# Optimization experiments

Hardware: AMD Instinct MI355X
Metric: run time of the kernel (lower is better)

Reference implementation:

```python
import jax, jax.numpy as jnp
import numpy as np

N_HEAD = 16
LN_EPS = 1e-5


def _rope_tables(T, hd, dtype):
    # Standard GPT-NeoX style rotary tables: cos/sin of shape [T, hd]
    inv = 1.0 / (10000.0 ** (np.arange(0, hd, 2, dtype=np.float64) / hd))
    freqs = np.outer(np.arange(T), inv)
    emb = np.concatenate([freqs, freqs], axis=-1)
    return jnp.asarray(np.cos(emb), dtype), jnp.asarray(np.sin(emb), dtype)


def _rotate_half(x):
    x1, x2 = jnp.split(x, 2, axis=-1)
    return jnp.concatenate([-x2, x1], axis=-1)


def _layernorm(x, g, b):
    mu = x.mean(-1, keepdims=True)
    var = x.var(-1, keepdims=True)
    return (x - mu) / jnp.sqrt(var + LN_EPS) * g + b


def _heads(x, H):
    B, T, C = x.shape
    return x.reshape(B, T, H, C // H).transpose(0, 2, 1, 3)  # [B,H,T,hd]


def _lin_attention(Q, K, V, causal):
    # Q,K,V: [B,H,T,hd]; ELU+1 feature map, RoPE on features, denom = sum_s Q.K
    Qf = jax.nn.elu(Q) + 1.0
    Kf = jax.nn.elu(K) + 1.0
    hd = Qf.shape[-1]
    cq, sq = _rope_tables(Qf.shape[2], hd, Qf.dtype)
    ck, sk = _rope_tables(Kf.shape[2], hd, Kf.dtype)
    Qr = Qf * cq + _rotate_half(Qf) * sq
    Kr = Kf * ck + _rotate_half(Kf) * sk
    # denom.sum(-1) == Qf . (sum_s Kf) -- avoid materializing a second TxS matrix
    denom = jnp.einsum('bhtd,bhd->bht', Qf, Kf.sum(axis=2))[..., None]
    att = jnp.einsum('bhtd,bhsd->bhts', Qr, Kr)
    if causal:
        T, S = att.shape[-2], att.shape[-1]
        att = jnp.where(jnp.tril(jnp.ones((T, S), dtype=bool)), att, 0.0)
    att = att / denom
    y = jnp.einsum('bhts,bhsd->bhtd', att, V)
    B, H, T, hd = y.shape
    return y.transpose(0, 2, 1, 3).reshape(B, T, H * hd)


def _forward(x, memory, ln1_g, ln1_b, sa_qkv_w, sa_qkv_b, sa_proj_w, sa_proj_b,
             ln2_g, ln2_b, ca_q_w, ca_q_b, ca_kv_w, ca_kv_b, ca_proj_w, ca_proj_b,
             ln3_g, ln3_b, fc_w, fc_b, fcp_w, fcp_b):
    H = N_HEAD
    # causal self-attention
    h = _layernorm(x, ln1_g, ln1_b)
    qkv = h @ sa_qkv_w + sa_qkv_b
    Q, K, V = jnp.split(qkv, 3, axis=-1)
    y = _lin_attention(_heads(Q, H), _heads(K, H), _heads(V, H), causal=True)
    x = x + (y @ sa_proj_w + sa_proj_b)
    # cross-attention
    h = _layernorm(x, ln2_g, ln2_b)
    q = h @ ca_q_w + ca_q_b
    kv = memory @ ca_kv_w + ca_kv_b
    K, V = jnp.split(kv, 2, axis=-1)
    y = _lin_attention(_heads(q, H), _heads(K, H), _heads(V, H), causal=False)
    x = x + (y @ ca_proj_w + ca_proj_b)
    # MLP with tanh-approx GELU
    h = _layernorm(x, ln3_g, ln3_b)
    h = jax.nn.gelu(h @ fc_w + fc_b, approximate=True)
    x = x + (h @ fcp_w + fcp_b)
    return x


def setup_inputs() -> dict:
    key = jax.random.key(0)
    ks = jax.random.split(key, 12)
    B, T, S, C = 2, 1024, 1024, 1024
    w = lambda k, shape: jax.random.normal(k, shape, dtype=jnp.float32) * 0.02
    return {
        'x': jax.random.normal(ks[0], (B, T, C), dtype=jnp.float32),
        'memory': jax.random.normal(ks[1], (B, S, C), dtype=jnp.float32),
        'ln1_g': jnp.ones((C,), jnp.float32), 'ln1_b': jnp.zeros((C,), jnp.float32),
        'sa_qkv_w': w(ks[2], (C, 3 * C)), 'sa_qkv_b': jnp.zeros((3 * C,), jnp.float32),
        'sa_proj_w': w(ks[3], (C, C)), 'sa_proj_b': jnp.zeros((C,), jnp.float32),
        'ln2_g': jnp.ones((C,), jnp.float32), 'ln2_b': jnp.zeros((C,), jnp.float32),
        'ca_q_w': w(ks[4], (C, C)), 'ca_q_b': jnp.zeros((C,), jnp.float32),
        'ca_kv_w': w(ks[5], (C, 2 * C)), 'ca_kv_b': jnp.zeros((2 * C,), jnp.float32),
        'ca_proj_w': w(ks[6], (C, C)), 'ca_proj_b': jnp.zeros((C,), jnp.float32),
        'ln3_g': jnp.ones((C,), jnp.float32), 'ln3_b': jnp.zeros((C,), jnp.float32),
        'fc_w': w(ks[7], (C, 4 * C)), 'fc_b': jnp.zeros((4 * C,), jnp.float32),
        'fcp_w': w(ks[8], (4 * C, C)), 'fcp_b': jnp.zeros((C,), jnp.float32),
    }


def reference(x, memory, ln1_g, ln1_b, sa_qkv_w, sa_qkv_b, sa_proj_w, sa_proj_b,
              ln2_g, ln2_b, ca_q_w, ca_q_b, ca_kv_w, ca_kv_b, ca_proj_w, ca_proj_b,
              ln3_g, ln3_b, fc_w, fc_b, fcp_w, fcp_b):
    return _forward(x, memory, ln1_g, ln1_b, sa_qkv_w, sa_qkv_b, sa_proj_w, sa_proj_b,
                    ln2_g, ln2_b, ca_q_w, ca_q_b, ca_kv_w, ca_kv_b, ca_proj_w, ca_proj_b,
                    ln3_g, ln3_b, fc_w, fc_b, fcp_w, fcp_b)
```

## Files before the change

### kernel.cpp

```cpp
#include <hip/hip_runtime.h>
#include <math.h>

#define BB 2
#define TT 1024
#define CC 1024
#define HH 16
#define HD 64
#define MM (BB*TT)

typedef unsigned short u16;
typedef unsigned int u32;
typedef short s16x8 __attribute__((ext_vector_type(8)));
typedef float f32x4 __attribute__((ext_vector_type(4)));

__device__ __forceinline__ u16 f2bf(float f) {
    u32 u = __builtin_bit_cast(u32, f);
    u += 0x7fffu + ((u >> 16) & 1u);
    return (u16)(u >> 16);
}
__device__ __forceinline__ float bf2f(u16 h) {
    return __builtin_bit_cast(float, ((u32)h) << 16);
}
__device__ __forceinline__ void gload16(const void* g, void* l) {
    __builtin_amdgcn_global_load_lds((const __attribute__((address_space(1))) u32*)g,
                                     (__attribute__((address_space(3))) u32*)l, 16, 0, 0);
}
__device__ __forceinline__ float gelu_tanh(float x) {
    float x3 = x * x * x;
    return 0.5f * x * (1.0f + tanhf(0.7978845608028654f * (x + 0.044715f * x3)));
}
__device__ __forceinline__ float elu1(float v) {
    return (v > 0.0f) ? v + 1.0f : expf(v);
}

__device__ __forceinline__ void wtile(const float* __restrict__ in, u16* __restrict__ out,
                                      int K, int N, int local, float (*tl)[65]) {
    int tilesX = N >> 6;
    int n0 = (local % tilesX) * 64, k0 = (local / tilesX) * 64;
    int c = threadIdx.x & 63, r4 = threadIdx.x >> 6;
    #pragma unroll
    for (int i = 0; i < 16; ++i) {
        int r = r4 * 16 + i;
        tl[r][c] = in[(size_t)(k0 + r) * N + n0 + c];
    }
    __syncthreads();
    #pragma unroll
    for (int i = 0; i < 16; ++i) {
        int r = r4 * 16 + i;
        out[(size_t)(n0 + r) * K + k0 + c] = f2bf(tl[c][r]);
    }
}

__global__ __launch_bounds__(256) void prep_kernel(
        const float* __restrict__ w_qkv, u16* __restrict__ t_qkv,
        const float* __restrict__ w_pr,  u16* __restrict__ t_pr,
        const float* __restrict__ w_caq, u16* __restrict__ t_caq,
        const float* __restrict__ w_cakv,u16* __restrict__ t_cakv,
        const float* __restrict__ w_capr,u16* __restrict__ t_capr,
        const float* __restrict__ w_fc,  u16* __restrict__ t_fc,
        const float* __restrict__ w_fcp, u16* __restrict__ t_fcp,
        const float* __restrict__ memF,  u16* __restrict__ memB,
        float* __restrict__ cosT, float* __restrict__ sinT,
        const float* __restrict__ x, const float* __restrict__ ln1_g,
        const float* __restrict__ ln1_b, u16* __restrict__ hB) {
    __shared__ float tl[64][65];
    int bid = blockIdx.x;
    if (bid < 768)        wtile(w_qkv,  t_qkv,  1024, 3072, bid, tl);
    else if (bid < 1024)  wtile(w_pr,   t_pr,   1024, 1024, bid - 768, tl);
    else if (bid < 1280)  wtile(w_caq,  t_caq,  1024, 1024, bid - 1024, tl);
    else if (bid < 1792)  wtile(w_cakv, t_cakv, 1024, 2048, bid - 1280, tl);
    else if (bid < 2048)  wtile(w_capr, t_capr, 1024, 1024, bid - 1792, tl);
    else if (bid < 3072)  wtile(w_fc,   t_fc,   1024, 4096, bid - 2048, tl);
    else if (bid < 4096)  wtile(w_fcp,  t_fcp,  4096, 1024, bid - 3072, tl);
    else if (bid < 6144) {
        int i = (bid - 4096) * 256 + threadIdx.x;
        float4 v = reinterpret_cast<const float4*>(memF)[i];
        uint2 p;
        p.x = (u32)f2bf(v.x) | ((u32)f2bf(v.y) << 16);
        p.y = (u32)f2bf(v.z) | ((u32)f2bf(v.w) << 16);
        reinterpret_cast<uint2*>(memB)[i] = p;
    } else if (bid < 6272) {
        int idx = (bid - 6144) * 256 + threadIdx.x;
        int t = idx >> 5, d = idx & 31;
        double inv = pow(10000.0, -((double)d) / 32.0);
        double ang = (double)t * inv;
        cosT[t * 32 + d] = (float)cos(ang);
        sinT[t * 32 + d] = (float)sin(ang);
    } else {
        int row = bid - 6272;
        float4 v = reinterpret_cast<const float4*>(x + (size_t)row * CC)[threadIdx.x];
        float s  = v.x + v.y + v.z + v.w;
        float sq = v.x*v.x + v.y*v.y + v.z*v.z + v.w*v.w;
        #pragma unroll
        for (int off = 32; off >= 1; off >>= 1) {
            s  += __shfl_down(s, off);
            sq += __shfl_down(sq, off);
        }
        __shared__ float ls[4], lsq[4];
        int wave = threadIdx.x >> 6, lane = threadIdx.x & 63;
        if (lane == 0) { ls[wave] = s; lsq[wave] = sq; }
        __syncthreads();
        s  = ls[0] + ls[1] + ls[2] + ls[3];
        sq = lsq[0] + lsq[1] + lsq[2] + lsq[3];
        float mean = s * (1.0f / CC);
        float var  = sq * (1.0f / CC) - mean * mean;
        float rstd = rsqrtf(var + 1e-5f);
        float4 gv = reinterpret_cast<const float4*>(ln1_g)[threadIdx.x];
        float4 bv = reinterpret_cast<const float4*>(ln1_b)[threadIdx.x];
        float o0 = (v.x - mean) * rstd * gv.x + bv.x;
        float o1 = (v.y - mean) * rstd * gv.y + bv.y;
        float o2 = (v.z - mean) * rstd * gv.z + bv.z;
        float o3 = (v.w - mean) * rstd * gv.w + bv.w;
        uint2 p;
        p.x = (u32)f2bf(o0) | ((u32)f2bf(o1) << 16);
        p.y = (u32)f2bf(o2) | ((u32)f2bf(o3) << 16);
        reinterpret_cast<uint2*>(hB + (size_t)row * CC)[threadIdx.x] = p;
    }
}

#define M_F32RES 0
#define M_GELU   1
#define M_QKV    2
#define M_PART   5
#define M_CAQKV  6

template <int MODE>
__device__ __forceinline__ void emit(int row, int col, float v,
                                     const float* __restrict__ res,
                                     float* __restrict__ oF, u16* __restrict__ o1,
                                     u16* __restrict__ o2, u16* __restrict__ o3, int N) {
    if constexpr (MODE == M_F32RES) {
        size_t o = (size_t)row * N + col;
        oF[o] = v + res[o];
    } else if constexpr (MODE == M_GELU) {
        o1[(size_t)row * N + col] = f2bf(gelu_tanh(v));
    } else {
        int b = row >> 10, t = row & 1023;
        if (col < 1024) {
            int h = col >> 6, d = col & 63;
            o1[(((size_t)(b * HH + h)) * TT + t) * HD + d] = f2bf(elu1(v));
        } else if (col < 2048) {
            int c = col - 1024, h = c >> 6, d = c & 63;
            o2[(((size_t)(b * HH + h)) * TT + t) * HD + d] = f2bf(elu1(v));
        } else {
            int c = col - 2048, h = c >> 6, d = c & 63;
            o3[(((size_t)(b * HH + h)) * TT + t) * HD + d] = f2bf(v);
        }
    }
}

template <int BM, int BN, int BK, int MODE, int SPLITK>
__global__ __launch_bounds__(512, 8) void gemm_bf16(const u16* __restrict__ A,
                                                    const u16* __restrict__ A2,
                                                    const u16* __restrict__ BT,
                                                    const u16* __restrict__ BT2,
                                                    const float* __restrict__ bias,
                                                    const float* __restrict__ bias2,
                                                    const float* __restrict__ res,
                                                    float* __restrict__ oF,
                                                    u16* __restrict__ o1,
                                                    u16* __restrict__ o2,
                                                    u16* __restrict__ o3,
                                                    float* __restrict__ ksumP,
                                                    int N, int K) {
    constexpr int WM = BM / 4, WN = BN / 2;
    constexpr int FI = WM / 16, FJ = WN / 16;
    constexpr int CH = BK / 8;
    constexpr int IA = BM * CH / 512;
    constexpr int IB = BN * CH / 512;
    __shared__ u16 As[BM * BK];
    __shared__ u16 Bs[BN * BK];
    int tid = threadIdx.x;
    int wave = tid >> 6, lane = tid & 63;
    int wr = wave >> 1, wc = wave & 1;
    int gx = gridDim.x, gy = gridDim.y;
    int lid = blockIdx.x + gx * blockIdx.y;
    int chunk = (gx * gy) >> 3;
    int swz = (lid & 7) * chunk + (lid >> 3);
    int bx = swz % gx, by = swz / gx;
    int row0 = by * BM, col0 = bx * BN;
    const u16* Ause = A;
    const u16* Buse = BT;
    const float* buse = bias;
    if constexpr (MODE == M_CAQKV) {
        if (col0 >= 1024) {
            Ause = A2;
            Buse = BT2 - (size_t)1024 * K;
            buse = bias2 - 1024;
        }
    }
    int kbeg = 0, kcnt = K;
    if constexpr (SPLITK > 1) { kcnt = K / SPLITK; kbeg = blockIdx.z * kcnt; }
    int kend = kbeg + kcnt;

    f32x4 acc[FI][FJ] = {};
    int lr = lane & 15;
    for (int kt = kbeg; kt < kend; kt += BK) {
        __syncthreads();
        #pragma unroll
        for (int i = 0; i < IA; ++i) {
            int s = tid + i * 512;
            int r = s / CH, kb = s % CH;
            int kbs = kb ^ (r & (CH - 1));
            gload16(Ause + (size_t)(row0 + r) * K + kt + kbs * 8, &As[s * 8]);
        }
        #pragma unroll
        for (int i = 0; i < IB; ++i) {
            int s = tid + i * 512;
            int r = s / CH, kb = s % CH;
            int kbs = kb ^ (r & (CH - 1));
            gload16(Buse + (size_t)(col0 + r) * K + kt + kbs * 8, &Bs[s * 8]);
        }
        __syncthreads();
        #pragma unroll
        for (int ks = 0; ks < BK / 32; ++ks) {
            s16x8 a[FI], b[FJ];
            int kc = ks * 4 + (lane >> 4);
            int sw = (kc ^ (lr & (CH - 1))) * 8;
            #pragma unroll
            for (int i = 0; i < FI; ++i)
                a[i] = *reinterpret_cast<const s16x8*>(&As[(wr * WM + i * 16 + lr) * BK + sw]);
            #pragma unroll
            for (int j = 0; j < FJ; ++j)
                b[j] = *reinterpret_cast<const s16x8*>(&Bs[(wc * WN + j * 16 + lr) * BK + sw]);
            __builtin_amdgcn_s_setprio(1);
            #pragma unroll
            for (int i = 0; i < FI; ++i)
                #pragma unroll
                for (int j = 0; j < FJ; ++j)
                    acc[i][j] = __builtin_amdgcn_mfma_f32_16x16x32_bf16(a[i], b[j], acc[i][j], 0, 0, 0);
            __builtin_amdgcn_s_setprio(0);
        }
    }
    int lr4 = (lane >> 4) * 4;
    if constexpr (MODE == M_PART) {
        size_t zoff = (size_t)blockIdx.z * (size_t)(gridDim.y * BM) * N;
        #pragma unroll
        for (int j = 0; j < FJ; ++j) {
            int col = col0 + wc * WN + j * 16 + lr;
            #pragma unroll
            for (int i = 0; i < FI; ++i)
                #pragma unroll
                for (int r = 0; r < 4; ++r) {
                    int row = row0 + wr * WM + i * 16 + lr4 + r;
                    oF[zoff + (size_t)row * N + col] = acc[i][j][r];
                }
        }
    } else {
        constexpr int EM = (MODE == M_CAQKV) ? M_QKV : MODE;
        #pragma unroll
        for (int j = 0; j < FJ; ++j) {
            int col = col0 + wc * WN + j * 16 + lr;
            float bi = buse[col];
            #pragma unroll
            for (int i = 0; i < FI; ++i)
                #pragma unroll
                for (int r = 0; r < 4; ++r) {
                    int row = row0 + wr * WM + i * 16 + lr4 + r;
                    emit<EM>(row, col, acc[i][j][r] + bi, res, oF, o1, o2, o3, N);
                }
        }
        if constexpr (MODE == M_QKV || MODE == M_CAQKV) {
            if (col0 >= 1024 && col0 < 2048) {
                float* scratch = (float*)As;
                float part[FJ];
                #pragma unroll
                for (int j = 0; j < FJ; ++j) {
                    int col = col0 + wc * WN + j * 16 + lr;
                    float bi = buse[col];
                    float p = 0.f;
                    #pragma unroll
                    for (int i = 0; i < FI; ++i)
                        #pragma unroll
                        for (int r = 0; r < 4; ++r)
                            p += elu1(acc[i][j][r] + bi);
                    part[j] = p;
                }
                __syncthreads();
                int contrib = wr * 4 + (lane >> 4);
                #pragma unroll
                for (int j = 0; j < FJ; ++j) {
                    int colLocal = wc * WN + j * 16 + lr;
                    scratch[colLocal * 16 + contrib] = part[j];
                }
                __syncthreads();
                if (tid < BN) {
                    float s = 0.f;
                    #pragma unroll
                    for (int c = 0; c < 16; ++c) s += scratch[tid * 16 + c];
                    ksumP[(size_t)by * 1024 + (col0 - 1024) + tid] = s;
                }
            }
        }
    }
}

template <int S>
__global__ __launch_bounds__(256) void reduce_res_kernel(const float* __restrict__ P,
                                                         const float* __restrict__ bias,
                                                         const float* __restrict__ res,
                                                         float* __restrict__ out,
                                                         int N, int total4) {
    int idx = blockIdx.x * 256 + threadIdx.x;
    if (idx >= total4) return;
    float4 b = reinterpret_cast<const float4*>(bias)[idx & (N / 4 - 1)];
    float4 r = reinterpret_cast<const float4*>(res)[idx];
    float4 a = {b.x + r.x, b.y + r.y, b.z + r.z, b.w + r.w};
    #pragma unroll
    for (int s = 0; s < S; ++s) {
        float4 p = reinterpret_cast<const float4*>(P)[(size_t)s * total4 + idx];
        a.x += p.x; a.y += p.y; a.z += p.z; a.w += p.w;
    }
    reinterpret_cast<float4*>(out)[idx] = a;
}

template <int S>
__global__ __launch_bounds__(256) void reduce_ln_kernel(const float* __restrict__ P,
                                                        const float* __restrict__ bias,
                                                        const float* __restrict__ res,
                                                        const float* __restrict__ g,
                                                        const float* __restrict__ bta,
                                                        float* __restrict__ out,
                                                        u16* __restrict__ hout) {
    int row = blockIdx.x;
    int t = threadIdx.x;
    const int total4 = MM * CC / 4;
    size_t ro4 = (size_t)row * 256 + t;
    float4 b = reinterpret_cast<const float4*>(bias)[t];
    float4 r = reinterpret_cast<const float4*>(res)[ro4];
    float4 a = {b.x + r.x, b.y + r.y, b.z + r.z, b.w + r.w};
    #pragma unroll
    for (int s = 0; s < S; ++s) {
        float4 p = reinterpret_cast<const float4*>(P)[(size_t)s * total4 + ro4];
        a.x += p.x; a.y += p.y; a.z += p.z; a.w += p.w;
    }
    reinterpret_cast<float4*>(out)[ro4] = a;
    float s1 = a.x + a.y + a.z + a.w;
    float sq = a.x*a.x + a.y*a.y + a.z*a.z + a.w*a.w;
    #pragma unroll
    for (int off = 32; off >= 1; off >>= 1) {
        s1 += __shfl_down(s1, off);
        sq += __shfl_down(sq, off);
    }
    __shared__ float ls[4], lsq[4];
    int wave = t >> 6, lane = t & 63;
    if (lane == 0) { ls[wave] = s1; lsq[wave] = sq; }
    __syncthreads();
    s1 = ls[0] + ls[1] + ls[2] + ls[3];
    sq = lsq[0] + lsq[1] + lsq[2] + lsq[3];
    float mean = s1 * (1.0f / CC);
    float var  = sq * (1.0f / CC) - mean * mean;
    float rstd = rsqrtf(var + 1e-5f);
    float4 gv = reinterpret_cast<const float4*>(g)[t];
    float4 bv = reinterpret_cast<const float4*>(bta)[t];
    float o0 = (a.x - mean) * rstd * gv.x + bv.x;
    float o1 = (a.y - mean) * rstd * gv.y + bv.y;
    float o2 = (a.z - mean) * rstd * gv.z + bv.z;
    float o3 = (a.w - mean) * rstd * gv.w + bv.w;
    uint2 pk;
    pk.x = (u32)f2bf(o0) | ((u32)f2bf(o1) << 16);
    pk.y = (u32)f2bf(o2) | ((u32)f2bf(o3) << 16);
    reinterpret_cast<uint2*>(hout + (size_t)row * CC)[t] = pk;
}

__device__ __forceinline__ void rope_row(u16* __restrict__ buf, int bh, int t, int q,
                                         const float* __restrict__ cosT,
                                         const float* __restrict__ sinT) {
    int d0 = q * 8;
    size_t base = ((size_t)bh * TT + t) * HD;
    s16x8 lo = *reinterpret_cast<const s16x8*>(&buf[base + d0]);
    s16x8 hi = *reinterpret_cast<const s16x8*>(&buf[base + 32 + d0]);
    const float4* cp = reinterpret_cast<const float4*>(&cosT[t * 32 + d0]);
    const float4* sp = reinterpret_cast<const float4*>(&sinT[t * 32 + d0]);
    float4 c0 = cp[0], c1 = cp[1], s0 = sp[0], s1 = sp[1];
    float cc[8] = {c0.x, c0.y, c0.z, c0.w, c1.x, c1.y, c1.z, c1.w};
    float ss[8] = {s0.x, s0.y, s0.z, s0.w, s1.x, s1.y, s1.z, s1.w};
    s16x8 nlo, nhi;
    #pragma unroll
    for (int e = 0; e < 8; ++e) {
        float l = bf2f((u16)lo[e]), h = bf2f((u16)hi[e]);
        nlo[e] = (short)f2bf(l * cc[e] - h * ss[e]);
        nhi[e] = (short)f2bf(h * cc[e] + l * ss[e]);
    }
    *reinterpret_cast<s16x8*>(&buf[base + d0]) = nlo;
    *reinterpret_cast<s16x8*>(&buf[base + 32 + d0]) = nhi;
}

__global__ __launch_bounds__(256) void denom_rope_kernel(u16* __restrict__ Qb,
                                                         u16* __restrict__ Kb,
                                                         const float* __restrict__ KsumP,
                                                         const float* __restrict__ cosT,
                                                         const float* __restrict__ sinT,
                                                         float* __restrict__ den) {
    int bid = blockIdx.x;
    if (bid < 1024) {
        int bh = bid >> 5;
        int b = bh >> 4, h = bh & 15;
        int t0 = (bid & 31) * 32;
        __shared__ float ks[64];
        if (threadIdx.x < 64) {
            float s = 0.f;
            #pragma unroll
            for (int rb = 0; rb < 8; ++rb)
                s += KsumP[(size_t)(b * 8 + rb) * 1024 + h * 64 + threadIdx.x];
            ks[threadIdx.x] = s;
        }
        __syncthreads();
        int wave = threadIdx.x >> 6, lane = threadIdx.x & 63;
        int rw = lane >> 3, lsub = lane & 7;
        int t = t0 + wave * 8 + rw;
        s16x8 q = *reinterpret_cast<const s16x8*>(&Qb[((size_t)bh * TT + t) * HD + lsub * 8]);
        float p = 0.f;
        #pragma unroll
        for (int e = 0; e < 8; ++e) p += bf2f((u16)q[e]) * ks[lsub * 8 + e];
        p += __shfl_xor(p, 1);
        p += __shfl_xor(p, 2);
        p += __shfl_xor(p, 4);
        if (lsub == 0) den[bh * TT + t] = p;
        __syncthreads();
        if (threadIdx.x < 128) {
            int row = threadIdx.x >> 2, qq = threadIdx.x & 3;
            rope_row(Qb, bh, t0 + row, qq, cosT, sinT);
        }
    } else {
        int g = (bid - 1024) * 256 + threadIdx.x;
        int qq = g & 3;
        int t = (g >> 2) & 1023;
        int bh = g >> 12;
        rope_row(Kb, bh, t, qq, cosT, sinT);
    }
}

#define APAD 72
__global__ __launch_bounds__(256) void attn_mfma(const u16* __restrict__ Qr,
                                                 const u16* __restrict__ Kr,
                                                 const u16* __restrict__ Vr,
                                                 const float* __restrict__ den,
                                                 u16* __restrict__ out, int causal) {
    __shared__ u16 Qs[64 * APAD];
    __shared__ u16 Ks[64 * APAD];
    __shared__ u16 Vs[64 * APAD];
    __shared__ u16 Ps[64 * APAD];
    int lid = blockIdx.x + gridDim.x * blockIdx.y;
    int chunk = (gridDim.x * gridDim.y) >> 3;
    int swz = (lid & 7) * chunk + (lid >> 3);
    int tile = swz % gridDim.x;
    int bh = swz / gridDim.x;
    int b = bh >> 4, h = bh & 15;
    int t0 = tile * 64;
    int tid = threadIdx.x, wave = tid >> 6, lane = tid & 63;
    #pragma unroll
    for (int i = 0; i < 2; ++i) {
        int s = tid + i * 256;
        int r = s >> 3, kb = s & 7;
        *reinterpret_cast<s16x8*>(&Qs[r * APAD + kb * 8]) =
            *reinterpret_cast<const s16x8*>(&Qr[((size_t)bh * TT + t0 + r) * HD + kb * 8]);
    }
    __syncthreads();
    int lr = lane & 15, lk = (lane >> 4) * 8;
    s16x8 qf0 = *reinterpret_cast<const s16x8*>(&Qs[(wave * 16 + lr) * APAD + lk]);
    s16x8 qf1 = *reinterpret_cast<const s16x8*>(&Qs[(wave * 16 + lr) * APAD + 32 + lk]);
    f32x4 accO[4] = {};
    int ntiles = causal ? (tile + 1) : (TT / 64);
    for (int st = 0; st < ntiles; ++st) {
        int s0 = st * 64;
        __syncthreads();
        #pragma unroll
        for (int i = 0; i < 2; ++i) {
            int s = tid + i * 256;
            int r = s >> 3, kb = s & 7;
            *reinterpret_cast<s16x8*>(&Ks[r * APAD + kb * 8]) =
                *reinterpret_cast<const s16x8*>(&Kr[((size_t)bh * TT + s0 + r) * HD + kb * 8]);
            s16x8 vv = *reinterpret_cast<const s16x8*>(&Vr[((size_t)bh * TT + s0 + r) * HD + kb * 8]);
            int sp = (((r >> 3) ^ kb) << 3) + (r & 7);
            #pragma unroll
            for (int e = 0; e < 8; ++e)
                Vs[(kb * 8 + e) * APAD + sp] = (u16)vv[e];
        }
        __syncthreads();
        f32x4 accS[4] = {};
        __builtin_amdgcn_s_setprio(1);
        #pragma unroll
        for (int j = 0; j < 4; ++j) {
            s16x8 kb0 = *reinterpret_cast<const s16x8*>(&Ks[(j * 16 + lr) * APAD + lk]);
            s16x8 kb1 = *reinterpret_cast<const s16x8*>(&Ks[(j * 16 + lr) * APAD + 32 + lk]);
            accS[j] = __builtin_amdgcn_mfma_f32_16x16x32_bf16(qf0, kb0, accS[j], 0, 0, 0);
            accS[j] = __builtin_amdgcn_mfma_f32_16x16x32_bf16(qf1, kb1, accS[j], 0, 0, 0);
        }
        __builtin_amdgcn_s_setprio(0);
        int tl = wave * 16 + (lane >> 4) * 4;
        #pragma unroll
        for (int j = 0; j < 4; ++j) {
            #pragma unroll
            for (int r = 0; r < 4; ++r) {
                float v = accS[j][r];
                if (causal && (s0 + j * 16 + lr > t0 + tl + r)) v = 0.f;
                Ps[(tl + r) * APAD + j * 16 + lr] = f2bf(v);
            }
        }
        __syncthreads();
        __builtin_amdgcn_s_setprio(1);
        #pragma unroll
        for (int ks = 0; ks < 2; ++ks) {
            s16x8 pa = *reinterpret_cast<const s16x8*>(&Ps[(wave * 16 + lr) * APAD + ks * 32 + lk]);
            #pragma unroll
            for (int j = 0; j < 4; ++j) {
                int d = j * 16 + lr;
                int c = ks * 4 + (lane >> 4);
                int cp = c ^ ((d >> 3) & 7);
                s16x8 vb = *reinterpret_cast<const s16x8*>(&Vs[d * APAD + cp * 8]);
                accO[j] = __builtin_amdgcn_mfma_f32_16x16x32_bf16(pa, vb, accO[j], 0, 0, 0);
            }
        }
        __builtin_amdgcn_s_setprio(0);
    }
    int tl = wave * 16 + (lane >> 4) * 4;
    float invd[4];
    #pragma unroll
    for (int r = 0; r < 4; ++r) invd[r] = 1.0f / den[bh * TT + t0 + tl + r];
    #pragma unroll
    for (int j = 0; j < 4; ++j)
        #pragma unroll
        for (int r = 0; r < 4; ++r)
            out[(size_t)(b * TT + t0 + tl + r) * CC + h * HD + j * 16 + lr] = f2bf(accO[j][r] * invd[r]);
}

extern "C" void kernel_launch(void* const* d_in, const int* in_sizes, int n_in,
                              void* d_out, int out_size, void* d_ws, size_t ws_size,
                              hipStream_t stream) {
    const float* x        = (const float*)d_in[0];
    const float* memory   = (const float*)d_in[1];
    const float* ln1_g    = (const float*)d_in[2];
    const float* ln1_b    = (const float*)d_in[3];
    const float* sa_qkv_w = (const float*)d_in[4];
    const float* sa_qkv_b = (const float*)d_in[5];
    const float* sa_pr_w  = (const float*)d_in[6];
    const float* sa_pr_b  = (const float*)d_in[7];
    const float* ln2_g    = (const float*)d_in[8];
    const float* ln2_b    = (const float*)d_in[9];
    const float* ca_q_w   = (const float*)d_in[10];
    const float* ca_q_b   = (const float*)d_in[11];
    const float* ca_kv_w  = (const float*)d_in[12];
    const float* ca_kv_b  = (const float*)d_in[13];
    const float* ca_pr_w  = (const float*)d_in[14];
    const float* ca_pr_b  = (const float*)d_in[15];
    const float* ln3_g    = (const float*)d_in[16];
    const float* ln3_b    = (const float*)d_in[17];
    const float* fc_w     = (const float*)d_in[18];
    const float* fc_b     = (const float*)d_in[19];
    const float* fcp_w    = (const float*)d_in[20];
    const float* fcp_b    = (const float*)d_in[21];
    float* out = (float*)d_out;
    char* wsb  = (char*)d_ws;

    const size_t MB = 1024 * 1024;
    u16* qkvT  = (u16*)wsb;
    u16* prT   = (u16*)(wsb + 6 * MB);
    u16* caqT  = (u16*)(wsb + 8 * MB);
    u16* cakvT = (u16*)(wsb + 10 * MB);
    u16* caprT = (u16*)(wsb + 14 * MB);
    u16* fcT   = (u16*)(wsb + 16 * MB);
    u16* fcpT  = (u16*)(wsb + 24 * MB);
    u16* memB  = (u16*)(wsb + 32 * MB);
    u16* hB    = (u16*)(wsb + 36 * MB);
    u16* h2B   = (u16*)(wsb + 40 * MB);
    u16* Qb    = (u16*)(wsb + 44 * MB);
    u16* Kb    = (u16*)(wsb + 48 * MB);
    u16* Vb    = (u16*)(wsb + 52 * MB);
    float* Pbuf = (float*)(wsb + 44 * MB);
    u16*   fcB   = (u16*)wsb;
    float* Pbuf4 = (float*)(wsb + 40 * MB);
    float* KsumP = (float*)(wsb + 76 * MB + 65536);
    float* den   = (float*)(wsb + 76 * MB + 131072);
    float* cosT  = (float*)(wsb + 76 * MB + 262144);
    float* sinT  = (float*)(wsb + 76 * MB + 393216);

    dim3 b256(256), b512(512);
    const int TOT4 = MM * CC / 4;

    prep_kernel<<<dim3(8320), b256, 0, stream>>>(
        sa_qkv_w, qkvT, sa_pr_w, prT, ca_q_w, caqT, ca_kv_w, cakvT,
        ca_pr_w, caprT, fc_w, fcT, fcp_w, fcpT, memory, memB, cosT, sinT,
        x, ln1_g, ln1_b, hB);

    gemm_bf16<128, 64, 128, M_QKV, 1><<<dim3(48, 16), b512, 0, stream>>>(
        hB, nullptr, qkvT, nullptr, sa_qkv_b, nullptr, nullptr,
        nullptr, Qb, Kb, Vb, KsumP, 3072, 1024);
    denom_rope_kernel<<<dim3(1536), b256, 0, stream>>>(Qb, Kb, KsumP, cosT, sinT, den);
    attn_mfma<<<dim3(16, 32), b256, 0, stream>>>(Qb, Kb, Vb, den, h2B, 1);
    gemm_bf16<64, 64, 128, M_PART, 2><<<dim3(16, 32, 2), b512, 0, stream>>>(
        h2B, nullptr, prT, nullptr, nullptr, nullptr, nullptr,
        Pbuf, nullptr, nullptr, nullptr, nullptr, 1024, 1024);
    reduce_ln_kernel<2><<<dim3(MM), b256, 0, stream>>>(Pbuf, sa_pr_b, x, ln2_g, ln2_b, out, hB);

    gemm_bf16<128, 64, 128, M_CAQKV, 1><<<dim3(48, 16), b512, 0, stream>>>(
        hB, memB, caqT, cakvT, ca_q_b, ca_kv_b, nullptr,
        nullptr, Qb, Kb, Vb, KsumP, 3072, 1024);
    denom_rope_kernel<<<dim3(1536), b256, 0, stream>>>(Qb, Kb, KsumP, cosT, sinT, den);
    attn_mfma<<<dim3(16, 32), b256, 0, stream>>>(Qb, Kb, Vb, den, h2B, 0);
    gemm_bf16<64, 64, 128, M_PART, 2><<<dim3(16, 32, 2), b512, 0, stream>>>(
        h2B, nullptr, caprT, nullptr, nullptr, nullptr, nullptr,
        Pbuf, nullptr, nullptr, nullptr, nullptr, 1024, 1024);
    reduce_ln_kernel<2><<<dim3(MM), b256, 0, stream>>>(Pbuf, ca_pr_b, out, ln3_g, ln3_b, out, hB);

    gemm_bf16<128, 64, 64, M_GELU, 1><<<dim3(64, 16), b512, 0, stream>>>(
        hB, nullptr, fcT, nullptr, fc_b, nullptr, nullptr,
        nullptr, fcB, nullptr, nullptr, nullptr, 4096, 1024);
    gemm_bf16<128, 64, 64, M_PART, 4><<<dim3(16, 16, 4), b512, 0, stream>>>(
        fcB, nullptr, fcpT, nullptr, nullptr, nullptr, nullptr,
        Pbuf4, nullptr, nullptr, nullptr, nullptr, 1024, 4096);
    reduce_res_kernel<4><<<dim3(TOT4 / 256), b256, 0, stream>>>(Pbuf4, fcp_b, out, out, 1024, TOT4);
}
```

Baseline: 224.0 us.

## Fuse denominator and RoPE into attention kernel, dropping separate denom_rope pass

Removes the standalone denom_rope kernel. The attention kernel now computes the Ksum-based denominator and applies RoPE to its Q tile in shared memory, and applies RoPE to each K tile as it is loaded. This saves two launches plus the global read/write round trip of Q and K. The cost is redundant RoPE work on K: each K tile is rotated once per query tile that visits it, which is up to 16x in the non-causal pass, and the K load path now has extra cos/sin loads and ALU inside the loop.

Measured after the change: 249.9 us. +11.6%, slower.

```diff
diff --git a/kernel.cpp b/kernel.cpp
--- a/kernel.cpp
+++ b/kernel.cpp
@@ -363,84 +363,20 @@
     reinterpret_cast<uint2*>(hout + (size_t)row * CC)[t] = pk;
 }
 
-__device__ __forceinline__ void rope_row(u16* __restrict__ buf, int bh, int t, int q,
-                                         const float* __restrict__ cosT,
-                                         const float* __restrict__ sinT) {
-    int d0 = q * 8;
-    size_t base = ((size_t)bh * TT + t) * HD;
-    s16x8 lo = *reinterpret_cast<const s16x8*>(&buf[base + d0]);
-    s16x8 hi = *reinterpret_cast<const s16x8*>(&buf[base + 32 + d0]);
-    const float4* cp = reinterpret_cast<const float4*>(&cosT[t * 32 + d0]);
-    const float4* sp = reinterpret_cast<const float4*>(&sinT[t * 32 + d0]);
-    float4 c0 = cp[0], c1 = cp[1], s0 = sp[0], s1 = sp[1];
-    float cc[8] = {c0.x, c0.y, c0.z, c0.w, c1.x, c1.y, c1.z, c1.w};
-    float ss[8] = {s0.x, s0.y, s0.z, s0.w, s1.x, s1.y, s1.z, s1.w};
-    s16x8 nlo, nhi;
-    #pragma unroll
-    for (int e = 0; e < 8; ++e) {
-        float l = bf2f((u16)lo[e]), h = bf2f((u16)hi[e]);
-        nlo[e] = (short)f2bf(l * cc[e] - h * ss[e]);
-        nhi[e] = (short)f2bf(h * cc[e] + l * ss[e]);
-    }
-    *reinterpret_cast<s16x8*>(&buf[base + d0]) = nlo;
-    *reinterpret_cast<s16x8*>(&buf[base + 32 + d0]) = nhi;
-}
-
-__global__ __launch_bounds__(256) void denom_rope_kernel(u16* __restrict__ Qb,
-                                                         u16* __restrict__ Kb,
-                                                         const float* __restrict__ KsumP,
-                                                         const float* __restrict__ cosT,
-                                                         const float* __restrict__ sinT,
-                                                         float* __restrict__ den) {
-    int bid = blockIdx.x;
-    if (bid < 1024) {
-        int bh = bid >> 5;
-        int b = bh >> 4, h = bh & 15;
-        int t0 = (bid & 31) * 32;
-        __shared__ float ks[64];
-        if (threadIdx.x < 64) {
-            float s = 0.f;
-            #pragma unroll
-            for (int rb = 0; rb < 8; ++rb)
-                s += KsumP[(size_t)(b * 8 + rb) * 1024 + h * 64 + threadIdx.x];
-            ks[threadIdx.x] = s;
-        }
-        __syncthreads();
-        int wave = threadIdx.x >> 6, lane = threadIdx.x & 63;
-        int rw = lane >> 3, lsub = lane & 7;
-        int t = t0 + wave * 8 + rw;
-        s16x8 q = *reinterpret_cast<const s16x8*>(&Qb[((size_t)bh * TT + t) * HD + lsub * 8]);
-        float p = 0.f;
-        #pragma unroll
-        for (int e = 0; e < 8; ++e) p += bf2f((u16)q[e]) * ks[lsub * 8 + e];
-        p += __shfl_xor(p, 1);
-        p += __shfl_xor(p, 2);
-        p += __shfl_xor(p, 4);
-        if (lsub == 0) den[bh * TT + t] = p;
-        __syncthreads();
-        if (threadIdx.x < 128) {
-            int row = threadIdx.x >> 2, qq = threadIdx.x & 3;
-            rope_row(Qb, bh, t0 + row, qq, cosT, sinT);
-        }
-    } else {
-        int g = (bid - 1024) * 256 + threadIdx.x;
-        int qq = g & 3;
-        int t = (g >> 2) & 1023;
-        int bh = g >> 12;
-        rope_row(Kb, bh, t, qq, cosT, sinT);
-    }
-}
-
 #define APAD 72
 __global__ __launch_bounds__(256) void attn_mfma(const u16* __restrict__ Qr,
                                                  const u16* __restrict__ Kr,
                                                  const u16* __restrict__ Vr,
-                                                 const float* __restrict__ den,
+                                                 const float* __restrict__ KsumP,
+                                                 const float* __restrict__ cosT,
+                                                 const float* __restrict__ sinT,
                                                  u16* __restrict__ out, int causal) {
     __shared__ u16 Qs[64 * APAD];
     __shared__ u16 Ks[64 * APAD];
     __shared__ u16 Vs[64 * APAD];
     __shared__ u16 Ps[64 * APAD];
+    __shared__ float ksS[64];
+    __shared__ float denL[64];
     int lid = blockIdx.x + gridDim.x * blockIdx.y;
     int chunk = (gridDim.x * gridDim.y) >> 3;
     int swz = (lid & 7) * chunk + (lid >> 3);
@@ -455,6 +391,43 @@
         int r = s >> 3, kb = s & 7;
         *reinterpret_cast<s16x8*>(&Qs[r * APAD + kb * 8]) =
             *reinterpret_cast<const s16x8*>(&Qr[((size_t)bh * TT + t0 + r) * HD + kb * 8]);
+    }
+    if (tid < 64) {
+        float s = 0.f;
+        #pragma unroll
+        for (int rb = 0; rb < 8; ++rb)
+            s += KsumP[(size_t)(b * 8 + rb) * 1024 + h * 64 + tid];
+        ksS[tid] = s;
+    }
+    __syncthreads();
+    {
+        int row = tid >> 2, q = tid & 3;
+        float p = 0.f;
+        #pragma unroll
+        for (int e = 0; e < 16; ++e)
+            p += bf2f(Qs[row * APAD + q * 16 + e]) * ksS[q * 16 + e];
+        p += __shfl_xor(p, 1);
+        p += __shfl_xor(p, 2);
+        if (q == 0) denL[row] = p;
+    }
+    __syncthreads();
+    {
+        int row = tid >> 2, q = tid & 3;
+        int d0 = q * 8;
+        int t = t0 + row;
+        const float4* cpt = reinterpret_cast<const float4*>(&cosT[t * 32 + d0]);
+        const float4* spt = reinterpret_cast<const float4*>(&sinT[t * 32 + d0]);
+        float4 c0 = cpt[0], c1 = cpt[1], f0 = spt[0], f1 = spt[1];
+        float cc[8] = {c0.x, c0.y, c0.z, c0.w, c1.x, c1.y, c1.z, c1.w};
+        float ss[8] = {f0.x, f0.y, f0.z, f0.w, f1.x, f1.y, f1.z, f1.w};
+        u16* lo = &Qs[row * APAD + d0];
+        u16* hi = &Qs[row * APAD + 32 + d0];
+        #pragma unroll
+        for (int e = 0; e < 8; ++e) {
+            float l = bf2f(lo[e]), hh = bf2f(hi[e]);
+            lo[e] = f2bf(l * cc[e] - hh * ss[e]);
+            hi[e] = f2bf(hh * cc[e] + l * ss[e]);
+        }
     }
     __syncthreads();
     int lr = lane & 15, lk = (lane >> 4) * 8;
@@ -469,13 +442,30 @@
         for (int i = 0; i < 2; ++i) {
             int s = tid + i * 256;
             int r = s >> 3, kb = s & 7;
-            *reinterpret_cast<s16x8*>(&Ks[r * APAD + kb * 8]) =
-                *reinterpret_cast<const s16x8*>(&Kr[((size_t)bh * TT + s0 + r) * HD + kb * 8]);
-            s16x8 vv = *reinterpret_cast<const s16x8*>(&Vr[((size_t)bh * TT + s0 + r) * HD + kb * 8]);
-            int sp = (((r >> 3) ^ kb) << 3) + (r & 7);
+            int t = s0 + r;
+            size_t kbase = ((size_t)bh * TT + t) * HD;
+            int dlo = (kb & 3) * 8;
+            s16x8 lo8 = *reinterpret_cast<const s16x8*>(&Kr[kbase + dlo]);
+            s16x8 hi8 = *reinterpret_cast<const s16x8*>(&Kr[kbase + 32 + dlo]);
+            const float4* cpt = reinterpret_cast<const float4*>(&cosT[t * 32 + dlo]);
+            const float4* spt = reinterpret_cast<const float4*>(&sinT[t * 32 + dlo]);
+            float4 c0 = cpt[0], c1 = cpt[1], f0 = spt[0], f1 = spt[1];
+            float cc[8] = {c0.x, c0.y, c0.z, c0.w, c1.x, c1.y, c1.z, c1.w};
+            float ss[8] = {f0.x, f0.y, f0.z, f0.w, f1.x, f1.y, f1.z, f1.w};
+            float sgn = (kb < 4) ? -1.f : 1.f;
+            s16x8 outv;
+            #pragma unroll
+            for (int e = 0; e < 8; ++e) {
+                float pr = bf2f((u16)((kb < 4) ? lo8[e] : hi8[e]));
+                float ot = bf2f((u16)((kb < 4) ? hi8[e] : lo8[e]));
+                outv[e] = (short)f2bf(pr * cc[e] + sgn * ot * ss[e]);
+            }
+            *reinterpret_cast<s16x8*>(&Ks[r * APAD + kb * 8]) = outv;
+            s16x8 vv = *reinterpret_cast<const s16x8*>(&Vr[kbase + kb * 8]);
+            int spos = (((r >> 3) ^ kb) << 3) + (r & 7);
             #pragma unroll
             for (int e = 0; e < 8; ++e)
-                Vs[(kb * 8 + e) * APAD + sp] = (u16)vv[e];
+                Vs[(kb * 8 + e) * APAD + spos] = (u16)vv[e];
         }
         __syncthreads();
         f32x4 accS[4] = {};
@@ -517,7 +507,7 @@
     int tl = wave * 16 + (lane >> 4) * 4;
     float invd[4];
     #pragma unroll
-    for (int r = 0; r < 4; ++r) invd[r] = 1.0f / den[bh * TT + t0 + tl + r];
+    for (int r = 0; r < 4; ++r) invd[r] = 1.0f / denL[tl + r];
     #pragma unroll
     for (int j = 0; j < 4; ++j)
         #pragma unroll
@@ -571,7 +561,6 @@
     u16*   fcB   = (u16*)wsb;
     float* Pbuf4 = (float*)(wsb + 40 * MB);
     float* KsumP = (float*)(wsb + 76 * MB + 65536);
-    float* den   = (float*)(wsb + 76 * MB + 131072);
     float* cosT  = (float*)(wsb + 76 * MB + 262144);
     float* sinT  = (float*)(wsb + 76 * MB + 393216);
 
@@ -586,8 +575,7 @@
     gemm_bf16<128, 64, 128, M_QKV, 1><<<dim3(48, 16), b512, 0, stream>>>(
         hB, nullptr, qkvT, nullptr, sa_qkv_b, nullptr, nullptr,
         nullptr, Qb, Kb, Vb, KsumP, 3072, 1024);
-    denom_rope_kernel<<<dim3(1536), b256, 0, stream>>>(Qb, Kb, KsumP, cosT, sinT, den);
-    attn_mfma<<<dim3(16, 32), b256, 0, stream>>>(Qb, Kb, Vb, den, h2B, 1);
+    attn_mfma<<<dim3(16, 32), b256, 0, stream>>>(Qb, Kb, Vb, KsumP, cosT, sinT, h2B, 1);
     gemm_bf16<64, 64, 128, M_PART, 2><<<dim3(16, 32, 2), b512, 0, stream>>>(
         h2B, nullptr, prT, nullptr, nullptr, nullptr, nullptr,
         Pbuf, nullptr, nullptr, nullptr, nullptr, 1024, 1024);
@@ -596,8 +584,7 @@
     gemm_bf16<128, 64, 128, M_CAQKV, 1><<<dim3(48, 16), b512, 0, stream>>>(
         hB, memB, caqT, cakvT, ca_q_b, ca_kv_b, nullptr,
         nullptr, Qb, Kb, Vb, KsumP, 3072, 1024);
-    denom_rope_kernel<<<dim3(1536), b256, 0, stream>>>(Qb, Kb, KsumP, cosT, sinT, den);
-    attn_mfma<<<dim3(16, 32), b256, 0, stream>>>(Qb, Kb, Vb, den, h2B, 0);
+    attn_mfma<<<dim3(16, 32), b256, 0, stream>>>(Qb, Kb, Vb, KsumP, cosT, sinT, h2B, 0);
     gemm_bf16<64, 64, 128, M_PART, 2><<<dim3(16, 32, 2), b512, 0, stream>>>(
         h2B, nullptr, caprT, nullptr, nullptr, nullptr, nullptr,
         Pbuf, nullptr, nullptr, nullptr, nullptr, 1024, 1024);
```
